# Optimization experiments

Hardware: AMD Instinct MI355X
Metric: run time of the kernel (lower is better)

## Reference

```python
import jax, jax.numpy as jnp
import numpy as np

KERNEL = 3  # kernel_size from init_kwargs


def _unfold(x, k):
    """torch.nn.functional.unfold with padding=k//2, stride=1.
    Returns [b, c*k*k, h*w] with torch's ordering: index = c*(k*k) + kh*k + kw.
    """
    b, c, h, w = x.shape
    p = k // 2
    xp = jnp.pad(x, ((0, 0), (0, 0), (p, p), (p, p)))
    # fixed k*k = 9 slices (small static loop, not a data-dim loop)
    cols = jnp.stack(
        [xp[:, :, i:i + h, j:j + w] for i in range(k) for j in range(k)],
        axis=2,
    )  # [b, c, k*k, h, w]
    return cols.reshape(b, c * k * k, h * w)


def setup_inputs() -> dict:
    key = jax.random.key(0)
    k1, k2 = jax.random.split(key)
    x = jax.random.normal(k1, (8, 64, 128, 128), dtype=jnp.float32)
    # memory parameter: torch.rand -> uniform [0, 1), shape [c*k*k, out_channels]
    memory = jax.random.uniform(k2, (64 * KERNEL * KERNEL, 128), dtype=jnp.float32)
    return {"x": x, "memory": memory}


def reference(x, memory):
    b, c, h, w = x.shape
    cols = _unfold(x, KERNEL)                 # [b, c*k*k, h*w]
    cols = jax.nn.softmax(cols, axis=1)       # softmax over unfolded patch dim
    out = jnp.einsum('ki,bkl->bil', memory, cols)  # [b, out_ch, h*w]
    return out.reshape(b, memory.shape[1], h, w)
```

## Files before the change

### kernel.cpp

```cpp
#include <hip/hip_runtime.h>
#include <stdint.h>


#define Cn 64
#define Hn 128
#define Wn 128
#define OC 128
#define HW (Hn * Wn)

typedef __attribute__((ext_vector_type(8))) short bf16x8_t;
typedef __attribute__((ext_vector_type(4))) float f32x4_t;
typedef __attribute__((ext_vector_type(16))) float f32x16_t;

__device__ inline unsigned short f2bf(float f) {
    union { float f; uint32_t u; } v; v.f = f;
    uint32_t u = v.u;
    u += 0x7fffu + ((u >> 16) & 1u);
    return (unsigned short)(u >> 16);
}
__device__ inline float bf2f(unsigned short h) {
    union { uint32_t u; float f; } v; v.u = ((uint32_t)h) << 16;
    return v.f;
}

__global__ void prep_b2(const float* __restrict__ mem, uint4* __restrict__ Bt2,
                        uint4* __restrict__ ones) {
    if (blockIdx.x == 36) {
        if (threadIdx.x < 8)
            ones[threadIdx.x] = make_uint4(0x3F803F80u, 0x3F803F80u, 0x3F803F80u, 0x3F803F80u);
        return;
    }
    int u = blockIdx.x * 256 + threadIdx.x;
    int n = u & 127;
    int cid = u >> 7;
    int hi = cid & 1;
    int kc = cid >> 1;
    int q = kc >> 2, cblk = kc & 3;
    unsigned short h8[8];
#pragma unroll
    for (int j = 0; j < 8; j++) {
        int c = cblk * 16 + hi * 8 + j;
        h8[j] = f2bf(mem[(c * 9 + q) * OC + n]);
    }
    Bt2[cid * 128 + n] = *(const uint4*)h8;
}

__global__ __launch_bounds__(256) void exp_tr3(const float* __restrict__ x,
                                               uint4* __restrict__ Etu,
                                               float* __restrict__ S) {
    __shared__ uint32_t lu[64 * 68];
    __shared__ float Spart[256];
    int bid = blockIdx.x;
    int b = bid >> 7, h = bid & 127;
    int t = threadIdx.x;
    int wv = t >> 6, lane = t & 63;

    const float* xr = x + (size_t)b * Cn * HW + h * Wn;
#pragma unroll
    for (int i = 0; i < 16; i++) {
        int c = i * 4 + wv;
        float2 v = *(const float2*)(xr + (size_t)c * HW + lane * 2);
        uint32_t pk = (uint32_t)f2bf(__expf(v.x)) | ((uint32_t)f2bf(__expf(v.y)) << 16);
        lu[c * 68 + lane] = pk;
    }
    __syncthreads();

    const unsigned short* Lp = (const unsigned short*)lu;
    int w = t & 127, ch0 = (t >> 7) * 32;
    unsigned short us[32];
    float s = 0.f;
#pragma unroll
    for (int j = 0; j < 32; j++) {
        unsigned short hb = Lp[(ch0 + j) * 136 + w];
        us[j] = hb;
        s += bf2f(hb);
    }
    size_t pix = (size_t)(b * Hn + h) * Wn + w;
    uint4* dst = Etu + pix * 8 + (t >> 7) * 4;
    const uint4* srcv = (const uint4*)us;
    dst[0] = srcv[0]; dst[1] = srcv[1]; dst[2] = srcv[2]; dst[3] = srcv[3];

    Spart[t] = s;
    __syncthreads();
    if (t < 128)
        S[pix] = Spart[t] + Spart[t + 128];
}

__global__ __launch_bounds__(256, 4) void conv3(const uint4* __restrict__ Etu,
                                                const uint4* __restrict__ Bt2,
                                                const float* __restrict__ S,
                                                const uint4* __restrict__ ones,
                                                float* __restrict__ out) {
    __shared__ __align__(16) uint4 EtL[180 * 8];
    __shared__ float Sh[180];
    __shared__ float Zt[128];

    int bid = blockIdx.x;
    int b = bid >> 7;
    int ty = (bid >> 3) & 15, tx = bid & 7;
    int h0 = ty * 8, w0 = tx * 16;
    int t = threadIdx.x;

    const uint4* Etb = Etu + (size_t)b * HW * 8;
#pragma unroll
    for (int i = 0; i < 6; i++) {
        int qd = i * 256 + t;
        if (qd < 1440) {
            int p = qd >> 3, slot = qd & 7;
            int py = p / 18, px = p - py * 18;
            int gy = h0 - 1 + py, gx = w0 - 1 + px;
            bool in = (gy >= 0) & (gy < Hn) & (gx >= 0) & (gx < Wn);
            int g = slot ^ (p & 7);
            const uint4* src = in ? (Etb + ((size_t)(gy * Wn + gx)) * 8 + g)
                                  : (ones + g);
            EtL[p * 8 + slot] = *src;
        }
    }
    if (t < 180) {
        int py = t / 18, px = t - py * 18;
        int gy = h0 - 1 + py, gx = w0 - 1 + px;
        bool in = (gy >= 0) & (gy < Hn) & (gx >= 0) & (gx < Wn);
        Sh[t] = in ? S[(size_t)b * HW + gy * Wn + gx] : 64.0f;
    }
    __syncthreads();

    if (t < 128) {
        int zy = t >> 4, zx = t & 15;
        float z = 0.f;
#pragma unroll
        for (int dy = 0; dy < 3; dy++)
#pragma unroll
            for (int dx = 0; dx < 3; dx++)
                z += Sh[(zy + dy) * 18 + (zx + dx)];
        Zt[t] = 1.0f / z;
    }
    __syncthreads();

    int lane = t & 63, wv = t >> 6;
    int l31 = lane & 31, hi = lane >> 5;
    int y0 = wv * 2 + (l31 >> 4);
    int x0 = l31 & 15;

    f32x16_t acc[4];
#pragma unroll
    for (int g = 0; g < 4; g++)
#pragma unroll
        for (int r = 0; r < 16; r++) acc[g][r] = 0.f;

    bf16x8_t Wf[2][4], Ef[2];

    auto loadW = [&](int kc, bf16x8_t* Wd) {
        const uint4* bp = Bt2 + (size_t)((kc * 2 + hi) * 128 + l31);
#pragma unroll
        for (int g = 0; g < 4; g++)
            Wd[g] = *(const bf16x8_t*)(bp + g * 32);
    };
    auto loadE = [&](int kc, bf16x8_t& Ed) {
        int q = kc >> 2, cblk = kc & 3;
        int kh = q / 3, kw = q - kh * 3;
        int pix = (y0 + kh) * 18 + (x0 + kw);
        int g = cblk * 2 + hi;
        Ed = *(const bf16x8_t*)&EtL[pix * 8 + (g ^ (pix & 7))];
    };

    loadW(0, Wf[0]);
    loadE(0, Ef[0]);
#pragma unroll
    for (int kc = 0; kc < 36; kc++) {
        int cur = kc & 1, nxt = cur ^ 1;
        if (kc + 1 < 36) {
            loadW(kc + 1, Wf[nxt]);
            loadE(kc + 1, Ef[nxt]);
        }
#pragma unroll
        for (int g = 0; g < 4; g++)
            acc[g] = __builtin_amdgcn_mfma_f32_32x32x16_bf16(Wf[cur][g], Ef[cur], acc[g], 0, 0, 0);
    }

    float zi = Zt[wv * 32 + l31];
    float* obase = out + (size_t)b * OC * HW + (h0 + y0) * Wn + (w0 + x0)
                 + (size_t)(4 * hi) * HW;
#pragma unroll
    for (int g = 0; g < 4; g++) {
#pragma unroll
        for (int r = 0; r < 16; r++) {
            int nrel = g * 32 + (r & 3) + 8 * (r >> 2);
            obase[(size_t)nrel * HW] = acc[g][r] * zi;
        }
    }
}

extern "C" void kernel_launch(void* const* d_in, const int* in_sizes, int n_in,
                              void* d_out, int out_size, void* d_ws, size_t ws_size,
                              hipStream_t stream) {
    const float* x = (const float*)d_in[0];
    const float* mem = (const float*)d_in[1];
    float* out = (float*)d_out;
    char* ws = (char*)d_ws;

    uint4* Etu = (uint4*)ws;
    float* S = (float*)(ws + 16777216);
    uint4* Bt2 = (uint4*)(ws + 17301504);
    uint4* ones = (uint4*)(ws + 17448960);

    prep_b2<<<37, 256, 0, stream>>>(mem, Bt2, ones);
    exp_tr3<<<1024, 256, 0, stream>>>(x, Etu, S);
    conv3<<<1024, 256, 0, stream>>>(Etu, Bt2, S, ones, out);
}
```

Before: 124.7 us.

## Enlarge conv tile to 16x16, reuse weight fragments, rework exp transpose

The conv kernel now computes a 16x16 pixel tile per block, so each wave holds two E fragments per k-step and reuses every loaded weight fragment for two MFMAs. This halves the global weight reads per output and shrinks the halo overhead, and the grid drops to 512 blocks. Prefetch is deepened to three stages, at the cost of more registers and lower occupancy (launch bounds 2). The exp/transpose kernel packs channel pairs during the first pass and computes partial sums there, which removes the second reduction barrier and the per-halfword LDS reads.

Measured after the change: 116.0 us. 1.07x faster.

```diff
diff --git a/kernel.cpp b/kernel.cpp
--- a/kernel.cpp
+++ b/kernel.cpp
@@ -18,8 +18,12 @@
     u += 0x7fffu + ((u >> 16) & 1u);
     return (unsigned short)(u >> 16);
 }
-__device__ inline float bf2f(unsigned short h) {
-    union { uint32_t u; float f; } v; v.u = ((uint32_t)h) << 16;
+__device__ inline float bf_lo(uint32_t u) {
+    union { uint32_t u; float f; } v; v.u = u << 16;
+    return v.f;
+}
+__device__ inline float bf_hi(uint32_t u) {
+    union { uint32_t u; float f; } v; v.u = u & 0xffff0000u;
     return v.f;
 }
 
@@ -45,67 +49,67 @@
     Bt2[cid * 128 + n] = *(const uint4*)h8;
 }
 
-__global__ __launch_bounds__(256) void exp_tr3(const float* __restrict__ x,
+__global__ __launch_bounds__(256) void exp_tr4(const float* __restrict__ x,
                                                uint4* __restrict__ Etu,
                                                float* __restrict__ S) {
-    __shared__ uint32_t lu[64 * 68];
-    __shared__ float Spart[256];
+    __shared__ uint32_t L[32 * 132];
+    __shared__ float Spart[512];
     int bid = blockIdx.x;
     int b = bid >> 7, h = bid & 127;
     int t = threadIdx.x;
     int wv = t >> 6, lane = t & 63;
 
     const float* xr = x + (size_t)b * Cn * HW + h * Wn;
-#pragma unroll
-    for (int i = 0; i < 16; i++) {
-        int c = i * 4 + wv;
-        float2 v = *(const float2*)(xr + (size_t)c * HW + lane * 2);
-        uint32_t pk = (uint32_t)f2bf(__expf(v.x)) | ((uint32_t)f2bf(__expf(v.y)) << 16);
-        lu[c * 68 + lane] = pk;
-    }
+    float s0 = 0.f, s1 = 0.f;
+#pragma unroll
+    for (int i = 0; i < 8; i++) {
+        int cp = wv * 8 + i;
+        const float* r0 = xr + (size_t)(2 * cp) * HW + 2 * lane;
+        float2 v0 = *(const float2*)r0;
+        float2 v1 = *(const float2*)(r0 + HW);
+        uint32_t p0 = (uint32_t)f2bf(__expf(v0.x)) | ((uint32_t)f2bf(__expf(v1.x)) << 16);
+        uint32_t p1 = (uint32_t)f2bf(__expf(v0.y)) | ((uint32_t)f2bf(__expf(v1.y)) << 16);
+        s0 += bf_lo(p0) + bf_hi(p0);
+        s1 += bf_lo(p1) + bf_hi(p1);
+        *(uint2*)&L[cp * 132 + 2 * lane] = make_uint2(p0, p1);
+    }
+    *(float2*)&Spart[wv * 128 + 2 * lane] = make_float2(s0, s1);
     __syncthreads();
 
-    const unsigned short* Lp = (const unsigned short*)lu;
-    int w = t & 127, ch0 = (t >> 7) * 32;
-    unsigned short us[32];
-    float s = 0.f;
-#pragma unroll
-    for (int j = 0; j < 32; j++) {
-        unsigned short hb = Lp[(ch0 + j) * 136 + w];
-        us[j] = hb;
-        s += bf2f(hb);
-    }
+    int w = t >> 1, half = t & 1;
+    uint32_t us[16];
+#pragma unroll
+    for (int j = 0; j < 16; j++)
+        us[j] = L[(half * 16 + j) * 132 + w];
     size_t pix = (size_t)(b * Hn + h) * Wn + w;
-    uint4* dst = Etu + pix * 8 + (t >> 7) * 4;
-    const uint4* srcv = (const uint4*)us;
-    dst[0] = srcv[0]; dst[1] = srcv[1]; dst[2] = srcv[2]; dst[3] = srcv[3];
-
-    Spart[t] = s;
-    __syncthreads();
-    if (t < 128)
-        S[pix] = Spart[t] + Spart[t + 128];
-}
-
-__global__ __launch_bounds__(256, 4) void conv3(const uint4* __restrict__ Etu,
+    uint4* dst = Etu + pix * 8 + half * 4;
+    const uint4* sv = (const uint4*)us;
+    dst[0] = sv[0]; dst[1] = sv[1]; dst[2] = sv[2]; dst[3] = sv[3];
+
+    if (half == 0)
+        S[pix] = Spart[w] + Spart[128 + w] + Spart[256 + w] + Spart[384 + w];
+}
+
+__global__ __launch_bounds__(256, 2) void conv4(const uint4* __restrict__ Etu,
                                                 const uint4* __restrict__ Bt2,
                                                 const float* __restrict__ S,
                                                 const uint4* __restrict__ ones,
                                                 float* __restrict__ out) {
-    __shared__ __align__(16) uint4 EtL[180 * 8];
-    __shared__ float Sh[180];
-    __shared__ float Zt[128];
+    __shared__ __align__(16) uint4 EtL[324 * 8];
+    __shared__ float Sh[324];
+    __shared__ float Zt[256];
 
     int bid = blockIdx.x;
-    int b = bid >> 7;
-    int ty = (bid >> 3) & 15, tx = bid & 7;
-    int h0 = ty * 8, w0 = tx * 16;
+    int b = bid >> 6;
+    int ty = (bid >> 3) & 7, tx = bid & 7;
+    int h0 = ty * 16, w0 = tx * 16;
     int t = threadIdx.x;
 
     const uint4* Etb = Etu + (size_t)b * HW * 8;
 #pragma unroll
-    for (int i = 0; i < 6; i++) {
+    for (int i = 0; i < 11; i++) {
         int qd = i * 256 + t;
-        if (qd < 1440) {
+        if (qd < 2592) {
             int p = qd >> 3, slot = qd & 7;
             int py = p / 18, px = p - py * 18;
             int gy = h0 - 1 + py, gx = w0 - 1 + px;
@@ -116,15 +120,19 @@
             EtL[p * 8 + slot] = *src;
         }
     }
-    if (t < 180) {
-        int py = t / 18, px = t - py * 18;
-        int gy = h0 - 1 + py, gx = w0 - 1 + px;
-        bool in = (gy >= 0) & (gy < Hn) & (gx >= 0) & (gx < Wn);
-        Sh[t] = in ? S[(size_t)b * HW + gy * Wn + gx] : 64.0f;
+#pragma unroll
+    for (int i = 0; i < 2; i++) {
+        int p = i * 256 + t;
+        if (p < 324) {
+            int py = p / 18, px = p - py * 18;
+            int gy = h0 - 1 + py, gx = w0 - 1 + px;
+            bool in = (gy >= 0) & (gy < Hn) & (gx >= 0) & (gx < Wn);
+            Sh[p] = in ? S[(size_t)b * HW + gy * Wn + gx] : 64.0f;
+        }
     }
     __syncthreads();
 
-    if (t < 128) {
+    {
         int zy = t >> 4, zx = t & 15;
         float z = 0.f;
 #pragma unroll
@@ -138,54 +146,65 @@
 
     int lane = t & 63, wv = t >> 6;
     int l31 = lane & 31, hi = lane >> 5;
-    int y0 = wv * 2 + (l31 >> 4);
-    int x0 = l31 & 15;
-
-    f32x16_t acc[4];
-#pragma unroll
-    for (int g = 0; g < 4; g++)
-#pragma unroll
-        for (int r = 0; r < 16; r++) acc[g][r] = 0.f;
-
-    bf16x8_t Wf[2][4], Ef[2];
-
-    auto loadW = [&](int kc, bf16x8_t* Wd) {
+    int x0v = l31 & 15;
+    int y0[2];
+    y0[0] = (wv * 2 + 0) * 2 + (l31 >> 4);
+    y0[1] = (wv * 2 + 1) * 2 + (l31 >> 4);
+
+    f32x16_t acc[2][4];
+#pragma unroll
+    for (int j = 0; j < 2; j++)
+#pragma unroll
+        for (int g = 0; g < 4; g++)
+#pragma unroll
+            for (int r = 0; r < 16; r++) acc[j][g][r] = 0.f;
+
+    bf16x8_t Wf[3][4], Ef[3][2];
+
+    auto loadW = [&](int kc, int s) {
         const uint4* bp = Bt2 + (size_t)((kc * 2 + hi) * 128 + l31);
 #pragma unroll
         for (int g = 0; g < 4; g++)
-            Wd[g] = *(const bf16x8_t*)(bp + g * 32);
+            Wf[s][g] = *(const bf16x8_t*)(bp + g * 32);
     };
-    auto loadE = [&](int kc, bf16x8_t& Ed) {
+    auto loadE = [&](int kc, int s) {
         int q = kc >> 2, cblk = kc & 3;
         int kh = q / 3, kw = q - kh * 3;
-        int pix = (y0 + kh) * 18 + (x0 + kw);
         int g = cblk * 2 + hi;
-        Ed = *(const bf16x8_t*)&EtL[pix * 8 + (g ^ (pix & 7))];
+#pragma unroll
+        for (int j = 0; j < 2; j++) {
+            int pix = (y0[j] + kh) * 18 + (x0v + kw);
+            Ef[s][j] = *(const bf16x8_t*)&EtL[pix * 8 + (g ^ (pix & 7))];
+        }
     };
 
-    loadW(0, Wf[0]);
-    loadE(0, Ef[0]);
+    loadW(0, 0); loadE(0, 0);
+    loadW(1, 1); loadE(1, 1);
+    loadW(2, 2); loadE(2, 2);
 #pragma unroll
     for (int kc = 0; kc < 36; kc++) {
-        int cur = kc & 1, nxt = cur ^ 1;
-        if (kc + 1 < 36) {
-            loadW(kc + 1, Wf[nxt]);
-            loadE(kc + 1, Ef[nxt]);
-        }
+        int s = kc % 3;
 #pragma unroll
         for (int g = 0; g < 4; g++)
-            acc[g] = __builtin_amdgcn_mfma_f32_32x32x16_bf16(Wf[cur][g], Ef[cur], acc[g], 0, 0, 0);
-    }
-
-    float zi = Zt[wv * 32 + l31];
-    float* obase = out + (size_t)b * OC * HW + (h0 + y0) * Wn + (w0 + x0)
-                 + (size_t)(4 * hi) * HW;
-#pragma unroll
-    for (int g = 0; g < 4; g++) {
-#pragma unroll
-        for (int r = 0; r < 16; r++) {
-            int nrel = g * 32 + (r & 3) + 8 * (r >> 2);
-            obase[(size_t)nrel * HW] = acc[g][r] * zi;
+#pragma unroll
+            for (int j = 0; j < 2; j++)
+                acc[j][g] = __builtin_amdgcn_mfma_f32_32x32x16_bf16(
+                    Wf[s][g], Ef[s][j], acc[j][g], 0, 0, 0);
+        if (kc + 3 < 36) { loadW(kc + 3, s); loadE(kc + 3, s); }
+    }
+
+#pragma unroll
+    for (int j = 0; j < 2; j++) {
+        float zi = Zt[(wv * 2 + j) * 32 + l31];
+        float* ob = out + (size_t)b * OC * HW + (h0 + y0[j]) * Wn + (w0 + x0v)
+                  + (size_t)(4 * hi) * HW;
+#pragma unroll
+        for (int g = 0; g < 4; g++) {
+#pragma unroll
+            for (int r = 0; r < 16; r++) {
+                int nrel = g * 32 + (r & 3) + 8 * (r >> 2);
+                ob[(size_t)nrel * HW] = acc[j][g][r] * zi;
+            }
         }
     }
 }
@@ -204,6 +223,6 @@
     uint4* ones = (uint4*)(ws + 17448960);
 
     prep_b2<<<37, 256, 0, stream>>>(mem, Bt2, ones);
-    exp_tr3<<<1024, 256, 0, stream>>>(x, Etu, S);
-    conv3<<<1024, 256, 0, stream>>>(Etu, Bt2, S, ones, out);
-}
+    exp_tr4<<<1024, 256, 0, stream>>>(x, Etu, S);
+    conv4<<<512, 256, 0, stream>>>(Etu, Bt2, S, ones, out);
+}
```
